# Kernel optimization log

Hardware: AMD Instinct MI355X
Metric: run time of the kernel (lower is better)

The kernel has to match this reference:

```python
import jax, jax.numpy as jnp
import numpy as np

B, N, G, D, H = 32, 512, 512, 512, 16
KD = D // H            # key_dim = embedding_dim // head_num
CLIP = 10.0            # tanh logit clipping


def _heads(x):
    # [B, C, D] -> [B, H, C, KD]
    b, c, _ = x.shape
    return x.reshape(b, c, H, KD).transpose(0, 2, 1, 3)


def setup_inputs() -> dict:
    key = jax.random.key(0)
    ks = jax.random.split(key, 9)
    s = 0.02
    return {
        "encoded_nodes": jax.random.normal(ks[0], (B, N, D), jnp.float32),
        "encoded_last": jax.random.normal(ks[1], (B, G, D), jnp.float32),
        "group_ninf_mask": jnp.zeros((B, G, N), jnp.float32),
        "Wq_graph": jax.random.normal(ks[2], (D, D), jnp.float32) * s,
        "Wq_first": jax.random.normal(ks[3], (D, D), jnp.float32) * s,
        "Wq_last": jax.random.normal(ks[4], (D, D), jnp.float32) * s,
        "Wk": jax.random.normal(ks[5], (D, D), jnp.float32) * s,
        "Wv": jax.random.normal(ks[6], (D, D), jnp.float32) * s,
        "Wcomb": jax.random.normal(ks[7], (D, D), jnp.float32) * s,
        "bcomb": jnp.zeros((D,), jnp.float32),
    }


def reference(encoded_nodes, encoded_last, group_ninf_mask,
              Wq_graph, Wq_first, Wq_last, Wk, Wv, Wcomb, bcomb):
    # reset(): graph embedding = mean over nodes, keys/values from encoded_nodes
    graph = encoded_nodes.mean(axis=1, keepdims=True)            # [B,1,D]
    q = (_heads(graph @ Wq_graph.T)                              # [B,H,1,KD] broadcast
         + _heads(encoded_last @ Wq_first.T)                     # q_first (first call)
         + _heads(encoded_last @ Wq_last.T))                     # [B,H,G,KD]
    k = _heads(encoded_nodes @ Wk.T)                             # [B,H,N,KD]
    v = _heads(encoded_nodes @ Wv.T)                             # [B,H,N,KD]

    # stage 1: masked multi-head attention
    score = jnp.einsum('bhgk,bhnk->bhgn', q, k) / float(np.sqrt(KD))
    score = score + group_ninf_mask[:, None, :, :]
    w = jax.nn.softmax(score, axis=-1)
    out = jnp.einsum('bhgn,bhnk->bhgk', w, v)
    out = out.transpose(0, 2, 1, 3).reshape(-1, G, D)            # [B,G,D]
    mh = out @ Wcomb.T + bcomb

    # stage 2: single-head score -> scale -> tanh clip -> mask -> softmax
    s2 = jnp.einsum('bgd,bnd->bgn', mh, encoded_nodes) / float(np.sqrt(D))
    s2 = CLIP * jnp.tanh(s2) + group_ninf_mask
    return jax.nn.softmax(s2, axis=-1)
```

## Files before the change

kernel.cpp:

```cpp
#include <hip/hip_runtime.h>
#include <hip/hip_bf16.h>
#include <stdint.h>
#include <math.h>

#define B_  32
#define N_  512
#define G_  512
#define D_  512
#define H_  16
#define KD_ 32

using bf16x8 = __attribute__((ext_vector_type(8))) short;
using f32x4  = __attribute__((ext_vector_type(4))) float;
typedef unsigned short u16;

__device__ __forceinline__ u16 f2b(float x) {
  union { __hip_bfloat16 h; u16 u; } c;
  c.h = __float2bfloat16(x);
  return c.u;
}
__device__ __forceinline__ float b2f(u16 u) {
  union { float f; unsigned int i; } c;
  c.i = ((unsigned int)u) << 16;
  return c.f;
}

__device__ __forceinline__ void async16(void* lds, const void* g) {
  __builtin_amdgcn_global_load_lds(
      (const __attribute__((address_space(1))) unsigned int*)(uintptr_t)g,
      (__attribute__((address_space(3))) unsigned int*)(uintptr_t)lds,
      16, 0, 0);
}

__global__ __launch_bounds__(512) void mean_split_kernel(
    const float* __restrict__ enc, u16* __restrict__ hi, u16* __restrict__ lo,
    float* __restrict__ partial)
{
  const int b  = blockIdx.x;
  const int nc = blockIdx.y;
  const int d  = threadIdx.x;
  const size_t base = ((size_t)b * N_ + (size_t)nc * 64) * D_ + d;
  float psum = 0.f;
  for (int i = 0; i < 64; ++i) {
    float v = enc[base + (size_t)i * D_];
    psum += v;
    u16 h = f2b(v);
    hi[base + (size_t)i * D_] = h;
    lo[base + (size_t)i * D_] = f2b(v - b2f(h));
  }
  partial[((size_t)b * 8 + nc) * D_ + d] = psum;
}

__global__ __launch_bounds__(512) void mean_final_kernel(
    const float* __restrict__ partial, float* __restrict__ graph)
{
  const int b = blockIdx.x, d = threadIdx.x;
  float s = 0.f;
  for (int c = 0; c < 8; ++c) s += partial[((size_t)b * 8 + c) * D_ + d];
  graph[b * D_ + d] = s * (1.0f / N_);
}

__global__ void split4_kernel(const float* __restrict__ in,
                              u16* __restrict__ hi, u16* __restrict__ lo, int n4)
{
  int i = blockIdx.x * blockDim.x + threadIdx.x;
  if (i < n4) {
    float4 v = ((const float4*)in)[i];
    ushort4 h, l;
    h.x = f2b(v.x); l.x = f2b(v.x - b2f(h.x));
    h.y = f2b(v.y); l.y = f2b(v.y - b2f(h.y));
    h.z = f2b(v.z); l.z = f2b(v.z - b2f(h.z));
    h.w = f2b(v.w); l.w = f2b(v.w - b2f(h.w));
    ((ushort4*)hi)[i] = h;
    ((ushort4*)lo)[i] = l;
  }
}

__global__ void wsum_split_kernel(const float* __restrict__ a, const float* __restrict__ b,
                                  u16* __restrict__ hi, u16* __restrict__ lo, int n4)
{
  int i = blockIdx.x * blockDim.x + threadIdx.x;
  if (i < n4) {
    float4 va = ((const float4*)a)[i];
    float4 vb = ((const float4*)b)[i];
    float x0 = va.x + vb.x, x1 = va.y + vb.y, x2 = va.z + vb.z, x3 = va.w + vb.w;
    ushort4 h, l;
    h.x = f2b(x0); l.x = f2b(x0 - b2f(h.x));
    h.y = f2b(x1); l.y = f2b(x1 - b2f(h.y));
    h.z = f2b(x2); l.z = f2b(x2 - b2f(h.z));
    h.w = f2b(x3); l.w = f2b(x3 - b2f(h.w));
    ((ushort4*)hi)[i] = h;
    ((ushort4*)lo)[i] = l;
  }
}

__global__ __launch_bounds__(256) void qg_kernel(
    const float* __restrict__ graph, const float* __restrict__ Wq,
    float* __restrict__ qg)
{
  const int b  = blockIdx.y;
  const int dd = blockIdx.x * 256 + threadIdx.x;
  const float* g = graph + b * D_;
  const float* w = Wq + (size_t)dd * D_;
  float s = 0.f;
  for (int k = 0; k < D_; ++k) s += g[k] * w[k];
  qg[b * D_ + dd] = s;
}

__global__ __launch_bounds__(256) void rowmax_kernel(
    const float* __restrict__ mask, float* __restrict__ rmx)
{
  const int row  = blockIdx.x * 4 + (threadIdx.x >> 6);
  const int lane = threadIdx.x & 63;
  const float* r = mask + (size_t)row * N_;
  float4 a  = *(const float4*)&r[lane * 8];
  float4 b4 = *(const float4*)&r[lane * 8 + 4];
  float m = fmaxf(fmaxf(fmaxf(a.x, a.y), fmaxf(a.z, a.w)),
                  fmaxf(fmaxf(b4.x, b4.y), fmaxf(b4.z, b4.w)));
#pragma unroll
  for (int w = 1; w < 64; w <<= 1) m = fmaxf(m, __shfl_xor(m, w));
  if (lane == 0) rmx[row] = m;
}

__global__ __launch_bounds__(64) void kmax_kernel(
    const u16* __restrict__ kvhi, float* __restrict__ kmx)
{
  const int b = blockIdx.x >> 4, h = blockIdx.x & 15;
  const int lane = threadIdx.x;
  float mx = 0.f;
  for (int i = 0; i < 8; ++i) {
    const int n = i * 64 + lane;
    const unsigned int* p =
        (const unsigned int*)&kvhi[((size_t)b * 512 + n) * 1024 + h * 32];
    float s = 0.f;
#pragma unroll
    for (int w = 0; w < 16; ++w) {
      unsigned int u = p[w];
      float f0 = __uint_as_float(u << 16);
      float f1 = __uint_as_float(u & 0xffff0000u);
      s = fmaf(f0, f0, s);
      s = fmaf(f1, f1, s);
    }
    mx = fmaxf(mx, s);
  }
#pragma unroll
  for (int w = 1; w < 64; w <<= 1) mx = fmaxf(mx, __shfl_xor(mx, w));
  if (lane == 0) kmx[blockIdx.x] = sqrtf(mx) * 1.01f;
}

__global__ __launch_bounds__(256) void vtrans_kernel(
    const u16* __restrict__ kvhi, const u16* __restrict__ kvlo,
    u16* __restrict__ vThi, u16* __restrict__ vTlo)
{
  const int b = blockIdx.x >> 4, h = blockIdx.x & 15;
  for (int d = 0; d < 32; ++d) {
#pragma unroll
    for (int c = 0; c < 2; ++c) {
      const int n = c * 256 + threadIdx.x;
      const size_t src = ((size_t)(b * 512 + n)) * 1024 + 512 + h * 32 + d;
      const size_t dst = (((size_t)b * 16 + h) * 32 + d) * 512 + n;
      vThi[dst] = kvhi[src];
      vTlo[dst] = kvlo[src];
    }
  }
}

template<int OUTMODE, int BIASMODE>
__global__ __launch_bounds__(256) void gemm_split_kernel(
    const u16* __restrict__ Ahi, const u16* __restrict__ Alo,
    const u16* __restrict__ Bhi, const u16* __restrict__ Blo,
    void* __restrict__ Chi, void* __restrict__ Clo,
    const float* __restrict__ bias,
    int M, int N, int K, long sA, long sB, long sC)
{
  __shared__ __align__(16) u16 AhS[4096], AlS[4096], BhS[4096], BlS[4096];

  const int z = blockIdx.z;
  Ahi += (size_t)z * sA; Alo += (size_t)z * sA;
  Bhi += (size_t)z * sB; Blo += (size_t)z * sB;

  const int brow = blockIdx.y * 128;
  const int bcol = blockIdx.x * 128;
  const int tid  = threadIdx.x;
  const int wid  = tid >> 6;
  const int lane = tid & 63;
  const int wr = wid >> 1, wc = wid & 1;

  f32x4 acc[4][4] = {};

  const int c0   = wid * 2;
  const int srow = lane >> 2;
  const int skk  = (lane & 3) * 8;

  const size_t g0 = (size_t)(brow + c0 * 16      + srow) * K + skk;
  const size_t g1 = (size_t)(brow + c0 * 16 + 16 + srow) * K + skk;
  const size_t h0 = (size_t)(bcol + c0 * 16      + srow) * K + skk;
  const size_t h1 = (size_t)(bcol + c0 * 16 + 16 + srow) * K + skk;
  u16* lA0 = &AhS[c0 * 512]; u16* lA1 = &AhS[c0 * 512 + 512];
  u16* la0 = &AlS[c0 * 512]; u16* la1 = &AlS[c0 * 512 + 512];
  u16* lB0 = &BhS[c0 * 512]; u16* lB1 = &BhS[c0 * 512 + 512];
  u16* lb0 = &BlS[c0 * 512]; u16* lb1 = &BlS[c0 * 512 + 512];

  const int aoff = (wr * 64 + (lane & 15)) * 32 + (lane >> 4) * 8;
  const int boff = (wc * 64 + (lane & 15)) * 32 + (lane >> 4) * 8;

  for (int k0 = 0; k0 < K; k0 += 32) {
    async16(lA0, Ahi + g0 + k0);
    async16(lA1, Ahi + g1 + k0);
    async16(la0, Alo + g0 + k0);
    async16(la1, Alo + g1 + k0);
    async16(lB0, Bhi + h0 + k0);
    async16(lB1, Bhi + h1 + k0);
    async16(lb0, Blo + h0 + k0);
    async16(lb1, Blo + h1 + k0);
    __syncthreads();

    bf16x8 ah[4], al[4], bh[4], bl[4];
#pragma unroll
    for (int m = 0; m < 4; ++m) {
      ah[m] = *(const bf16x8*)&AhS[aoff + m * 512];
      al[m] = *(const bf16x8*)&AlS[aoff + m * 512];
    }
#pragma unroll
    for (int n = 0; n < 4; ++n) {
      bh[n] = *(const bf16x8*)&BhS[boff + n * 512];
      bl[n] = *(const bf16x8*)&BlS[boff + n * 512];
    }
#pragma unroll
    for (int m = 0; m < 4; ++m)
#pragma unroll
      for (int n = 0; n < 4; ++n) {
        f32x4 t = acc[m][n];
        t = __builtin_amdgcn_mfma_f32_16x16x32_bf16(al[m], bh[n], t, 0, 0, 0);
        t = __builtin_amdgcn_mfma_f32_16x16x32_bf16(ah[m], bl[n], t, 0, 0, 0);
        t = __builtin_amdgcn_mfma_f32_16x16x32_bf16(ah[m], bh[n], t, 0, 0, 0);
        acc[m][n] = t;
      }
    __syncthreads();
  }

  const int r0 = brow + wr * 64 + (lane >> 4) * 4;
  const int cbase = bcol + wc * 64 + (lane & 15);
#pragma unroll
  for (int m = 0; m < 4; ++m) {
#pragma unroll
    for (int n = 0; n < 4; ++n) {
      const int c = cbase + n * 16;
#pragma unroll
      for (int j = 0; j < 4; ++j) {
        const int r = r0 + m * 16 + j;
        float v = acc[m][n][j];
        if (BIASMODE == 1) v += bias[(r >> 9) * 512 + c];
        if (BIASMODE == 2) v += bias[c];
        if (OUTMODE == 0) {
          ((float*)Chi)[(size_t)z * sC + (size_t)r * N + c] = v;
        } else {
          u16 h = f2b(v);
          ((u16*)Chi)[(size_t)r * N + c] = h;
          ((u16*)Clo)[(size_t)r * N + c] = f2b(v - b2f(h));
        }
      }
    }
  }
}

__global__ __launch_bounds__(256) void attn_mfma3_kernel(
    u16* __restrict__ Qhi, u16* __restrict__ Qlo,
    const u16* __restrict__ KVhi, const u16* __restrict__ KVlo,
    const u16* __restrict__ VThi, const u16* __restrict__ VTlo,
    const float* __restrict__ mask,
    const float* __restrict__ rowmaxb,
    const float* __restrict__ kmaxb)
{
  __shared__ __align__(16) u16 Ph[4][32][56], Pl[4][32][56];

  const int tid = threadIdx.x, wid = tid >> 6, lane = tid & 63;
  const int id   = blockIdx.x;
  const int h    = id & 15;
  const int gblk = (id >> 4) & 3;
  const int b    = id >> 6;
  const int g0   = gblk * 128 + wid * 32;
  const int colq = lane & 15, rowg = lane >> 4;

  const size_t qb = ((size_t)b * G_ + g0) * D_ + h * KD_;
  const size_t kb = (size_t)b * N_ * 1024 + h * KD_;
  const size_t vb = (((size_t)b * H_ + h) * KD_) * (size_t)N_;
  const float* Mb = mask + ((size_t)b * G_ + g0) * N_;

  bf16x8 qh[2], ql[2];
  qh[0] = *(const bf16x8*)&Qhi[qb + (size_t)colq * D_ + rowg * 8];
  ql[0] = *(const bf16x8*)&Qlo[qb + (size_t)colq * D_ + rowg * 8];
  qh[1] = *(const bf16x8*)&Qhi[qb + (size_t)(16 + colq) * D_ + rowg * 8];
  ql[1] = *(const bf16x8*)&Qlo[qb + (size_t)(16 + colq) * D_ + rowg * 8];

  const float scale = 0.17677669529663687f;
  const f32x4 zf = {0.f, 0.f, 0.f, 0.f};
  const bf16x8 ones = {0x3F80, 0x3F80, 0x3F80, 0x3F80, 0x3F80, 0x3F80, 0x3F80, 0x3F80};

  const float km = kmaxb[b * 16 + h];
  float nq2[2];
#pragma unroll
  for (int rf = 0; rf < 2; ++rf) {
    float s = 0.f;
    const unsigned int* qw = (const unsigned int*)&qh[rf];
#pragma unroll
    for (int w = 0; w < 4; ++w) {
      unsigned int u = qw[w];
      float f0 = __uint_as_float(u << 16);
      float f1 = __uint_as_float(u & 0xffff0000u);
      s = fmaf(f0, f0, s);
      s = fmaf(f1, f1, s);
    }
    s += __shfl_xor(s, 16);
    s += __shfl_xor(s, 32);
    nq2[rf] = s;
  }
  float mrow[2][4];
#pragma unroll
  for (int rf = 0; rf < 2; ++rf)
#pragma unroll
    for (int j = 0; j < 4; ++j) {
      const int r16 = rowg * 4 + j;
      float nq = sqrtf(__shfl(nq2[rf], r16)) * 1.01f;
      mrow[rf][j] = scale * nq * km + rowmaxb[(size_t)b * G_ + g0 + rf * 16 + r16];
    }

  f32x4 o[2][2] = {};
  f32x4 os[2] = {};

  for (int n0 = 0; n0 < N_; n0 += 32) {
    bf16x8 kh0 = *(const bf16x8*)&KVhi[kb + (size_t)(n0 + colq) * 1024 + rowg * 8];
    bf16x8 kl0 = *(const bf16x8*)&KVlo[kb + (size_t)(n0 + colq) * 1024 + rowg * 8];
    bf16x8 kh1 = *(const bf16x8*)&KVhi[kb + (size_t)(n0 + 16 + colq) * 1024 + rowg * 8];
    bf16x8 kl1 = *(const bf16x8*)&KVlo[kb + (size_t)(n0 + 16 + colq) * 1024 + rowg * 8];
    bf16x8 vh0 = *(const bf16x8*)&VThi[vb + (size_t)colq * N_ + n0 + rowg * 8];
    bf16x8 vl0 = *(const bf16x8*)&VTlo[vb + (size_t)colq * N_ + n0 + rowg * 8];
    bf16x8 vh1 = *(const bf16x8*)&VThi[vb + (size_t)(16 + colq) * N_ + n0 + rowg * 8];
    bf16x8 vl1 = *(const bf16x8*)&VTlo[vb + (size_t)(16 + colq) * N_ + n0 + rowg * 8];

#pragma unroll
    for (int rf = 0; rf < 2; ++rf) {
      f32x4 t0 = __builtin_amdgcn_mfma_f32_16x16x32_bf16(ql[rf], kh0, zf, 0, 0, 0);
      t0 = __builtin_amdgcn_mfma_f32_16x16x32_bf16(qh[rf], kl0, t0, 0, 0, 0);
      t0 = __builtin_amdgcn_mfma_f32_16x16x32_bf16(qh[rf], kh0, t0, 0, 0, 0);
      f32x4 t1 = __builtin_amdgcn_mfma_f32_16x16x32_bf16(ql[rf], kh1, zf, 0, 0, 0);
      t1 = __builtin_amdgcn_mfma_f32_16x16x32_bf16(qh[rf], kl1, t1, 0, 0, 0);
      t1 = __builtin_amdgcn_mfma_f32_16x16x32_bf16(qh[rf], kh1, t1, 0, 0, 0);
#pragma unroll
      for (int j = 0; j < 4; ++j) {
        const int gg = rf * 16 + rowg * 4 + j;
        float m0 = Mb[(size_t)gg * N_ + n0 + colq];
        float m1 = Mb[(size_t)gg * N_ + n0 + 16 + colq];
        float p0 = __expf(fmaf(t0[j], scale, m0 - mrow[rf][j]));
        float p1 = __expf(fmaf(t1[j], scale, m1 - mrow[rf][j]));
        unsigned int uh, ul;
        asm("v_cvt_pk_bf16_f32 %0, %1, %2" : "=v"(uh) : "v"(p0), "v"(p1));
        float h0f = __uint_as_float(uh << 16);
        float h1f = __uint_as_float(uh & 0xffff0000u);
        float l0 = p0 - h0f, l1 = p1 - h1f;
        asm("v_cvt_pk_bf16_f32 %0, %1, %2" : "=v"(ul) : "v"(l0), "v"(l1));
        Ph[wid][gg][colq]      = (u16)uh;
        Ph[wid][gg][16 + colq] = (u16)(uh >> 16);
        Pl[wid][gg][colq]      = (u16)ul;
        Pl[wid][gg][16 + colq] = (u16)(ul >> 16);
      }
    }
    asm volatile("s_waitcnt lgkmcnt(0)" ::: "memory");

    bf16x8 ph0 = *(const bf16x8*)&Ph[wid][colq][rowg * 8];
    bf16x8 pl0 = *(const bf16x8*)&Pl[wid][colq][rowg * 8];
    bf16x8 ph1 = *(const bf16x8*)&Ph[wid][16 + colq][rowg * 8];
    bf16x8 pl1 = *(const bf16x8*)&Pl[wid][16 + colq][rowg * 8];

    o[0][0] = __builtin_amdgcn_mfma_f32_16x16x32_bf16(pl0, vh0, o[0][0], 0, 0, 0);
    o[0][0] = __builtin_amdgcn_mfma_f32_16x16x32_bf16(ph0, vl0, o[0][0], 0, 0, 0);
    o[0][0] = __builtin_amdgcn_mfma_f32_16x16x32_bf16(ph0, vh0, o[0][0], 0, 0, 0);
    o[0][1] = __builtin_amdgcn_mfma_f32_16x16x32_bf16(pl0, vh1, o[0][1], 0, 0, 0);
    o[0][1] = __builtin_amdgcn_mfma_f32_16x16x32_bf16(ph0, vl1, o[0][1], 0, 0, 0);
    o[0][1] = __builtin_amdgcn_mfma_f32_16x16x32_bf16(ph0, vh1, o[0][1], 0, 0, 0);
    o[1][0] = __builtin_amdgcn_mfma_f32_16x16x32_bf16(pl1, vh0, o[1][0], 0, 0, 0);
    o[1][0] = __builtin_amdgcn_mfma_f32_16x16x32_bf16(ph1, vl0, o[1][0], 0, 0, 0);
    o[1][0] = __builtin_amdgcn_mfma_f32_16x16x32_bf16(ph1, vh0, o[1][0], 0, 0, 0);
    o[1][1] = __builtin_amdgcn_mfma_f32_16x16x32_bf16(pl1, vh1, o[1][1], 0, 0, 0);
    o[1][1] = __builtin_amdgcn_mfma_f32_16x16x32_bf16(ph1, vl1, o[1][1], 0, 0, 0);
    o[1][1] = __builtin_amdgcn_mfma_f32_16x16x32_bf16(ph1, vh1, o[1][1], 0, 0, 0);
    os[0] = __builtin_amdgcn_mfma_f32_16x16x32_bf16(ph0, ones, os[0], 0, 0, 0);
    os[0] = __builtin_amdgcn_mfma_f32_16x16x32_bf16(pl0, ones, os[0], 0, 0, 0);
    os[1] = __builtin_amdgcn_mfma_f32_16x16x32_bf16(ph1, ones, os[1], 0, 0, 0);
    os[1] = __builtin_amdgcn_mfma_f32_16x16x32_bf16(pl1, ones, os[1], 0, 0, 0);
  }

#pragma unroll
  for (int rf = 0; rf < 2; ++rf)
#pragma unroll
    for (int j = 0; j < 4; ++j) {
      const float inv = 1.f / os[rf][j];
      const int gg = rf * 16 + rowg * 4 + j;
      float v0 = o[rf][0][j] * inv;
      float v1 = o[rf][1][j] * inv;
      u16 h0 = f2b(v0), h1 = f2b(v1);
      Qhi[qb + (size_t)gg * D_ + colq]      = h0;
      Qlo[qb + (size_t)gg * D_ + colq]      = f2b(v0 - b2f(h0));
      Qhi[qb + (size_t)gg * D_ + 16 + colq] = h1;
      Qlo[qb + (size_t)gg * D_ + 16 + colq] = f2b(v1 - b2f(h1));
    }
}

__global__ __launch_bounds__(256) void softmax2_kernel(
    float* __restrict__ S, const float* __restrict__ mask)
{
  const int row  = blockIdx.x * 4 + (threadIdx.x >> 6);
  const int lane = threadIdx.x & 63;
  float* r = S + (size_t)row * N_;
  const float* mk = mask + (size_t)row * N_;
  const float iscale = 0.04419417382415922f;

  float4 a  = *(const float4*)&r[lane * 8];
  float4 b4 = *(const float4*)&r[lane * 8 + 4];
  float4 ma = *(const float4*)&mk[lane * 8];
  float4 mb = *(const float4*)&mk[lane * 8 + 4];

  float v[8] = {a.x, a.y, a.z, a.w, b4.x, b4.y, b4.z, b4.w};
  float m[8] = {ma.x, ma.y, ma.z, ma.w, mb.x, mb.y, mb.z, mb.w};

#pragma unroll
  for (int i = 0; i < 8; ++i) {
    float x  = v[i] * iscale;
    float e2 = __expf(2.f * x);
    float t  = 1.f - 2.f / (e2 + 1.f);
    v[i] = 10.f * t + m[i];
  }
  float mx = v[0];
#pragma unroll
  for (int i = 1; i < 8; ++i) mx = fmaxf(mx, v[i]);
#pragma unroll
  for (int w = 1; w < 64; w <<= 1) mx = fmaxf(mx, __shfl_xor(mx, w));
  float sum = 0.f;
#pragma unroll
  for (int i = 0; i < 8; ++i) { v[i] = __expf(v[i] - mx); sum += v[i]; }
#pragma unroll
  for (int w = 1; w < 64; w <<= 1) sum += __shfl_xor(sum, w);
  const float inv = 1.f / sum;

  float4 oa = {v[0] * inv, v[1] * inv, v[2] * inv, v[3] * inv};
  float4 ob = {v[4] * inv, v[5] * inv, v[6] * inv, v[7] * inv};
  *(float4*)&r[lane * 8]     = oa;
  *(float4*)&r[lane * 8 + 4] = ob;
}

extern "C" void kernel_launch(void* const* d_in, const int* in_sizes, int n_in,
                              void* d_out, int out_size, void* d_ws, size_t ws_size,
                              hipStream_t stream)
{
  const float* enc_nodes = (const float*)d_in[0];
  const float* enc_last  = (const float*)d_in[1];
  const float* mask      = (const float*)d_in[2];
  const float* Wq_graph  = (const float*)d_in[3];
  const float* Wq_first  = (const float*)d_in[4];
  const float* Wq_last   = (const float*)d_in[5];
  const float* Wk        = (const float*)d_in[6];
  const float* Wv        = (const float*)d_in[7];
  const float* Wcomb     = (const float*)d_in[8];
  const float* bcomb     = (const float*)d_in[9];
  float* out = (float*)d_out;

  char* ws = (char*)d_ws;
  size_t off = 0;
  auto alloc = [&](size_t bytes) {
    void* p = ws + off;
    off += (bytes + 255) & ~(size_t)255;
    return p;
  };

  const size_t EL = (size_t)B_ * G_ * D_;
  u16* encNhi = (u16*)alloc(EL * 2);
  u16* encNlo = (u16*)alloc(EL * 2);
  u16* encLhi = (u16*)alloc(EL * 2);
  u16* encLlo = (u16*)alloc(EL * 2);
  u16* qhi    = (u16*)alloc(EL * 2);
  u16* qlo    = (u16*)alloc(EL * 2);
  u16* kvhi   = (u16*)alloc(EL * 4);
  u16* kvlo   = (u16*)alloc(EL * 4);
  u16* Wqlhi  = (u16*)alloc((size_t)D_ * D_ * 2);
  u16* Wqllo  = (u16*)alloc((size_t)D_ * D_ * 2);
  u16* Wkvhi  = (u16*)alloc((size_t)D_ * D_ * 4);
  u16* Wkvlo  = (u16*)alloc((size_t)D_ * D_ * 4);
  u16* Wchi   = (u16*)alloc((size_t)D_ * D_ * 2);
  u16* Wclo   = (u16*)alloc((size_t)D_ * D_ * 2);
  float* partial = (float*)alloc((size_t)B_ * 8 * D_ * 4);
  float* graph   = (float*)alloc((size_t)B_ * D_ * 4);
  float* qg      = (float*)alloc((size_t)B_ * D_ * 4);
  float* rowmaxb = (float*)alloc((size_t)B_ * G_ * 4);
  float* kmaxb   = (float*)alloc((size_t)B_ * H_ * 4);
  u16* vThi = encLhi; u16* vTlo = encLlo;
  u16* athi = qhi;    u16* atlo = qlo;
  u16* mhhi = kvhi;   u16* mhlo = kvlo;

  mean_split_kernel<<<dim3(32, 8), 512, 0, stream>>>(enc_nodes, encNhi, encNlo, partial);
  mean_final_kernel<<<dim3(32), 512, 0, stream>>>(partial, graph);
  split4_kernel<<<dim3(8192), 256, 0, stream>>>(enc_last, encLhi, encLlo, (int)(EL / 4));
  wsum_split_kernel<<<dim3(256), 256, 0, stream>>>(Wq_first, Wq_last, Wqlhi, Wqllo, 65536);
  split4_kernel<<<dim3(256), 256, 0, stream>>>(Wk, Wkvhi, Wkvlo, 65536);
  split4_kernel<<<dim3(256), 256, 0, stream>>>(Wv, Wkvhi + 262144, Wkvlo + 262144, 65536);
  split4_kernel<<<dim3(256), 256, 0, stream>>>(Wcomb, Wchi, Wclo, 65536);
  qg_kernel<<<dim3(2, 32), 256, 0, stream>>>(graph, Wq_graph, qg);
  rowmax_kernel<<<dim3(4096), 256, 0, stream>>>(mask, rowmaxb);

  gemm_split_kernel<1, 1><<<dim3(4, 128, 1), 256, 0, stream>>>(
      encLhi, encLlo, Wqlhi, Wqllo, qhi, qlo, qg, 16384, 512, 512, 0, 0, 0);
  gemm_split_kernel<1, 0><<<dim3(8, 128, 1), 256, 0, stream>>>(
      encNhi, encNlo, Wkvhi, Wkvlo, kvhi, kvlo, nullptr, 16384, 1024, 512, 0, 0, 0);
  vtrans_kernel<<<dim3(512), 256, 0, stream>>>(kvhi, kvlo, vThi, vTlo);
  kmax_kernel<<<dim3(512), 64, 0, stream>>>(kvhi, kmaxb);

  attn_mfma3_kernel<<<dim3(2048), 256, 0, stream>>>(
      qhi, qlo, kvhi, kvlo, vThi, vTlo, mask, rowmaxb, kmaxb);

  gemm_split_kernel<1, 2><<<dim3(4, 128, 1), 256, 0, stream>>>(
      athi, atlo, Wchi, Wclo, mhhi, mhlo, bcomb, 16384, 512, 512, 0, 0, 0);
  gemm_split_kernel<0, 0><<<dim3(4, 4, 32), 256, 0, stream>>>(
      mhhi, mhlo, encNhi, encNlo, out, nullptr, nullptr, 512, 512, 512,
      262144, 262144, 262144);

  softmax2_kernel<<<dim3(4096), 256, 0, stream>>>(out, mask);
}
```

Baseline: 494.8 us.

## Fuse V transpose into KV GEMM epilogue and pipeline attention loop

The K/V projection GEMM epilogue now writes K to a compact buffer and V directly in transposed per-head layout, removing the separate transpose kernel and its extra memory pass. The attention kernel is software-pipelined with double-buffered K/V/mask registers and P shared-memory tiles, so the next tile's loads and QK-softmax overlap the current PV MFMAs. This costs more registers and makes the V stores from the GEMM uncoalesced.

```diff
diff --git a/kernel.cpp b/kernel.cpp
--- a/kernel.cpp
+++ b/kernel.cpp
@@ -123,7 +123,7 @@
 }
 
 __global__ __launch_bounds__(64) void kmax_kernel(
-    const u16* __restrict__ kvhi, float* __restrict__ kmx)
+    const u16* __restrict__ khi, float* __restrict__ kmx)
 {
   const int b = blockIdx.x >> 4, h = blockIdx.x & 15;
   const int lane = threadIdx.x;
@@ -131,7 +131,7 @@
   for (int i = 0; i < 8; ++i) {
     const int n = i * 64 + lane;
     const unsigned int* p =
-        (const unsigned int*)&kvhi[((size_t)b * 512 + n) * 1024 + h * 32];
+        (const unsigned int*)&khi[((size_t)b * 512 + n) * 512 + h * 32];
     float s = 0.f;
 #pragma unroll
     for (int w = 0; w < 16; ++w) {
@@ -148,28 +148,12 @@
   if (lane == 0) kmx[blockIdx.x] = sqrtf(mx) * 1.01f;
 }
 
-__global__ __launch_bounds__(256) void vtrans_kernel(
-    const u16* __restrict__ kvhi, const u16* __restrict__ kvlo,
-    u16* __restrict__ vThi, u16* __restrict__ vTlo)
-{
-  const int b = blockIdx.x >> 4, h = blockIdx.x & 15;
-  for (int d = 0; d < 32; ++d) {
-#pragma unroll
-    for (int c = 0; c < 2; ++c) {
-      const int n = c * 256 + threadIdx.x;
-      const size_t src = ((size_t)(b * 512 + n)) * 1024 + 512 + h * 32 + d;
-      const size_t dst = (((size_t)b * 16 + h) * 32 + d) * 512 + n;
-      vThi[dst] = kvhi[src];
-      vTlo[dst] = kvlo[src];
-    }
-  }
-}
-
 template<int OUTMODE, int BIASMODE>
 __global__ __launch_bounds__(256) void gemm_split_kernel(
     const u16* __restrict__ Ahi, const u16* __restrict__ Alo,
     const u16* __restrict__ Bhi, const u16* __restrict__ Blo,
     void* __restrict__ Chi, void* __restrict__ Clo,
+    void* __restrict__ Dhi, void* __restrict__ Dlo,
     const float* __restrict__ bias,
     int M, int N, int K, long sA, long sB, long sC)
 {
@@ -254,25 +238,37 @@
         if (BIASMODE == 2) v += bias[c];
         if (OUTMODE == 0) {
           ((float*)Chi)[(size_t)z * sC + (size_t)r * N + c] = v;
-        } else {
+        } else if (OUTMODE == 1) {
           u16 h = f2b(v);
           ((u16*)Chi)[(size_t)r * N + c] = h;
           ((u16*)Clo)[(size_t)r * N + c] = f2b(v - b2f(h));
+        } else {
+          u16 hv = f2b(v);
+          u16 lv = f2b(v - b2f(hv));
+          if (c < 512) {
+            ((u16*)Chi)[(size_t)r * 512 + c] = hv;
+            ((u16*)Clo)[(size_t)r * 512 + c] = lv;
+          } else {
+            const int bb = r >> 9, nn = r & 511, hh = (c >> 5) & 15, dd = c & 31;
+            const size_t idx = (((size_t)bb * 16 + hh) * 32 + dd) * 512 + nn;
+            ((u16*)Dhi)[idx] = hv;
+            ((u16*)Dlo)[idx] = lv;
+          }
         }
       }
     }
   }
 }
 
-__global__ __launch_bounds__(256) void attn_mfma3_kernel(
+__global__ __launch_bounds__(256) void attn_mfma4_kernel(
     u16* __restrict__ Qhi, u16* __restrict__ Qlo,
-    const u16* __restrict__ KVhi, const u16* __restrict__ KVlo,
+    const u16* __restrict__ Khi, const u16* __restrict__ Klo,
     const u16* __restrict__ VThi, const u16* __restrict__ VTlo,
     const float* __restrict__ mask,
     const float* __restrict__ rowmaxb,
     const float* __restrict__ kmaxb)
 {
-  __shared__ __align__(16) u16 Ph[4][32][56], Pl[4][32][56];
+  __shared__ __align__(16) u16 Ph[2][4][32][40], Pl[2][4][32][40];
 
   const int tid = threadIdx.x, wid = tid >> 6, lane = tid & 63;
   const int id   = blockIdx.x;
@@ -283,7 +279,7 @@
   const int colq = lane & 15, rowg = lane >> 4;
 
   const size_t qb = ((size_t)b * G_ + g0) * D_ + h * KD_;
-  const size_t kb = (size_t)b * N_ * 1024 + h * KD_;
+  const size_t kb = ((size_t)b * N_) * D_ + h * KD_;
   const size_t vb = (((size_t)b * H_ + h) * KD_) * (size_t)N_;
   const float* Mb = mask + ((size_t)b * G_ + g0) * N_;
 
@@ -296,6 +292,81 @@
   const float scale = 0.17677669529663687f;
   const f32x4 zf = {0.f, 0.f, 0.f, 0.f};
   const bf16x8 ones = {0x3F80, 0x3F80, 0x3F80, 0x3F80, 0x3F80, 0x3F80, 0x3F80, 0x3F80};
+
+  bf16x8 kh0[2], kl0[2], kh1[2], kl1[2];
+  bf16x8 vh0[2], vl0[2], vh1[2], vl1[2];
+  float  mm0[2][4], mm1[2][4];
+
+#define LOADK(s, n0_)                                                          \
+  kh0[s] = *(const bf16x8*)&Khi[kb + (size_t)((n0_) + colq) * D_ + rowg * 8];  \
+  kl0[s] = *(const bf16x8*)&Klo[kb + (size_t)((n0_) + colq) * D_ + rowg * 8];  \
+  kh1[s] = *(const bf16x8*)&Khi[kb + (size_t)((n0_) + 16 + colq) * D_ + rowg * 8]; \
+  kl1[s] = *(const bf16x8*)&Klo[kb + (size_t)((n0_) + 16 + colq) * D_ + rowg * 8];
+
+#define LOADV(s, n0_)                                                          \
+  vh0[s] = *(const bf16x8*)&VThi[vb + (size_t)colq * N_ + (n0_) + rowg * 8];   \
+  vl0[s] = *(const bf16x8*)&VTlo[vb + (size_t)colq * N_ + (n0_) + rowg * 8];   \
+  vh1[s] = *(const bf16x8*)&VThi[vb + (size_t)(16 + colq) * N_ + (n0_) + rowg * 8]; \
+  vl1[s] = *(const bf16x8*)&VTlo[vb + (size_t)(16 + colq) * N_ + (n0_) + rowg * 8];
+
+#define LOADM(n0_)                                                             \
+  _Pragma("unroll") for (int rf = 0; rf < 2; ++rf)                             \
+  _Pragma("unroll") for (int j = 0; j < 4; ++j) {                              \
+    const int gg = rf * 16 + rowg * 4 + j;                                     \
+    mm0[rf][j] = Mb[(size_t)gg * N_ + (n0_) + colq] - mrow[rf][j];             \
+    mm1[rf][j] = Mb[(size_t)gg * N_ + (n0_) + 16 + colq] - mrow[rf][j];        \
+  }
+
+#define QKSM(s, bb)                                                            \
+  _Pragma("unroll") for (int rf = 0; rf < 2; ++rf) {                           \
+    f32x4 t0 = __builtin_amdgcn_mfma_f32_16x16x32_bf16(ql[rf], kh0[s], zf, 0, 0, 0); \
+    t0 = __builtin_amdgcn_mfma_f32_16x16x32_bf16(qh[rf], kl0[s], t0, 0, 0, 0); \
+    t0 = __builtin_amdgcn_mfma_f32_16x16x32_bf16(qh[rf], kh0[s], t0, 0, 0, 0); \
+    f32x4 t1 = __builtin_amdgcn_mfma_f32_16x16x32_bf16(ql[rf], kh1[s], zf, 0, 0, 0); \
+    t1 = __builtin_amdgcn_mfma_f32_16x16x32_bf16(qh[rf], kl1[s], t1, 0, 0, 0); \
+    t1 = __builtin_amdgcn_mfma_f32_16x16x32_bf16(qh[rf], kh1[s], t1, 0, 0, 0); \
+    _Pragma("unroll") for (int j = 0; j < 4; ++j) {                            \
+      const int gg = rf * 16 + rowg * 4 + j;                                   \
+      float p0 = __expf(fmaf(t0[j], scale, mm0[rf][j]));                       \
+      float p1 = __expf(fmaf(t1[j], scale, mm1[rf][j]));                       \
+      unsigned int uh_, ul_;                                                   \
+      asm("v_cvt_pk_bf16_f32 %0, %1, %2" : "=v"(uh_) : "v"(p0), "v"(p1));      \
+      float h0f = __uint_as_float(uh_ << 16);                                  \
+      float h1f = __uint_as_float(uh_ & 0xffff0000u);                          \
+      float l0_ = p0 - h0f, l1_ = p1 - h1f;                                    \
+      asm("v_cvt_pk_bf16_f32 %0, %1, %2" : "=v"(ul_) : "v"(l0_), "v"(l1_));    \
+      Ph[bb][wid][gg][colq]      = (u16)uh_;                                   \
+      Ph[bb][wid][gg][16 + colq] = (u16)(uh_ >> 16);                           \
+      Pl[bb][wid][gg][colq]      = (u16)ul_;                                   \
+      Pl[bb][wid][gg][16 + colq] = (u16)(ul_ >> 16);                           \
+    }                                                                          \
+  }
+
+#define PVACC(s, bb) {                                                         \
+    bf16x8 ph0 = *(const bf16x8*)&Ph[bb][wid][colq][rowg * 8];                 \
+    bf16x8 pl0 = *(const bf16x8*)&Pl[bb][wid][colq][rowg * 8];                 \
+    bf16x8 ph1 = *(const bf16x8*)&Ph[bb][wid][16 + colq][rowg * 8];            \
+    bf16x8 pl1 = *(const bf16x8*)&Pl[bb][wid][16 + colq][rowg * 8];            \
+    o[0][0] = __builtin_amdgcn_mfma_f32_16x16x32_bf16(pl0, vh0[s], o[0][0], 0, 0, 0); \
+    o[0][0] = __builtin_amdgcn_mfma_f32_16x16x32_bf16(ph0, vl0[s], o[0][0], 0, 0, 0); \
+    o[0][0] = __builtin_amdgcn_mfma_f32_16x16x32_bf16(ph0, vh0[s], o[0][0], 0, 0, 0); \
+    o[0][1] = __builtin_amdgcn_mfma_f32_16x16x32_bf16(pl0, vh1[s], o[0][1], 0, 0, 0); \
+    o[0][1] = __builtin_amdgcn_mfma_f32_16x16x32_bf16(ph0, vl1[s], o[0][1], 0, 0, 0); \
+    o[0][1] = __builtin_amdgcn_mfma_f32_16x16x32_bf16(ph0, vh1[s], o[0][1], 0, 0, 0); \
+    o[1][0] = __builtin_amdgcn_mfma_f32_16x16x32_bf16(pl1, vh0[s], o[1][0], 0, 0, 0); \
+    o[1][0] = __builtin_amdgcn_mfma_f32_16x16x32_bf16(ph1, vl0[s], o[1][0], 0, 0, 0); \
+    o[1][0] = __builtin_amdgcn_mfma_f32_16x16x32_bf16(ph1, vh0[s], o[1][0], 0, 0, 0); \
+    o[1][1] = __builtin_amdgcn_mfma_f32_16x16x32_bf16(pl1, vh1[s], o[1][1], 0, 0, 0); \
+    o[1][1] = __builtin_amdgcn_mfma_f32_16x16x32_bf16(ph1, vl1[s], o[1][1], 0, 0, 0); \
+    o[1][1] = __builtin_amdgcn_mfma_f32_16x16x32_bf16(ph1, vh1[s], o[1][1], 0, 0, 0); \
+    os[0] = __builtin_amdgcn_mfma_f32_16x16x32_bf16(ph0, ones, os[0], 0, 0, 0); \
+    os[0] = __builtin_amdgcn_mfma_f32_16x16x32_bf16(pl0, ones, os[0], 0, 0, 0); \
+    os[1] = __builtin_amdgcn_mfma_f32_16x16x32_bf16(ph1, ones, os[1], 0, 0, 0); \
+    os[1] = __builtin_amdgcn_mfma_f32_16x16x32_bf16(pl1, ones, os[1], 0, 0, 0); \
+  }
+
+  LOADK(0, 0)
+  LOADV(0, 0)
 
   const float km = kmaxb[b * 16 + h];
   float nq2[2];
@@ -325,70 +396,33 @@
       mrow[rf][j] = scale * nq * km + rowmaxb[(size_t)b * G_ + g0 + rf * 16 + r16];
     }
 
+  LOADM(0)
+  QKSM(0, 0)
+
   f32x4 o[2][2] = {};
   f32x4 os[2] = {};
 
-  for (int n0 = 0; n0 < N_; n0 += 32) {
-    bf16x8 kh0 = *(const bf16x8*)&KVhi[kb + (size_t)(n0 + colq) * 1024 + rowg * 8];
-    bf16x8 kl0 = *(const bf16x8*)&KVlo[kb + (size_t)(n0 + colq) * 1024 + rowg * 8];
-    bf16x8 kh1 = *(const bf16x8*)&KVhi[kb + (size_t)(n0 + 16 + colq) * 1024 + rowg * 8];
-    bf16x8 kl1 = *(const bf16x8*)&KVlo[kb + (size_t)(n0 + 16 + colq) * 1024 + rowg * 8];
-    bf16x8 vh0 = *(const bf16x8*)&VThi[vb + (size_t)colq * N_ + n0 + rowg * 8];
-    bf16x8 vl0 = *(const bf16x8*)&VTlo[vb + (size_t)colq * N_ + n0 + rowg * 8];
-    bf16x8 vh1 = *(const bf16x8*)&VThi[vb + (size_t)(16 + colq) * N_ + n0 + rowg * 8];
-    bf16x8 vl1 = *(const bf16x8*)&VTlo[vb + (size_t)(16 + colq) * N_ + n0 + rowg * 8];
-
-#pragma unroll
-    for (int rf = 0; rf < 2; ++rf) {
-      f32x4 t0 = __builtin_amdgcn_mfma_f32_16x16x32_bf16(ql[rf], kh0, zf, 0, 0, 0);
-      t0 = __builtin_amdgcn_mfma_f32_16x16x32_bf16(qh[rf], kl0, t0, 0, 0, 0);
-      t0 = __builtin_amdgcn_mfma_f32_16x16x32_bf16(qh[rf], kh0, t0, 0, 0, 0);
-      f32x4 t1 = __builtin_amdgcn_mfma_f32_16x16x32_bf16(ql[rf], kh1, zf, 0, 0, 0);
-      t1 = __builtin_amdgcn_mfma_f32_16x16x32_bf16(qh[rf], kl1, t1, 0, 0, 0);
-      t1 = __builtin_amdgcn_mfma_f32_16x16x32_bf16(qh[rf], kh1, t1, 0, 0, 0);
-#pragma unroll
-      for (int j = 0; j < 4; ++j) {
-        const int gg = rf * 16 + rowg * 4 + j;
-        float m0 = Mb[(size_t)gg * N_ + n0 + colq];
-        float m1 = Mb[(size_t)gg * N_ + n0 + 16 + colq];
-        float p0 = __expf(fmaf(t0[j], scale, m0 - mrow[rf][j]));
-        float p1 = __expf(fmaf(t1[j], scale, m1 - mrow[rf][j]));
-        unsigned int uh, ul;
-        asm("v_cvt_pk_bf16_f32 %0, %1, %2" : "=v"(uh) : "v"(p0), "v"(p1));
-        float h0f = __uint_as_float(uh << 16);
-        float h1f = __uint_as_float(uh & 0xffff0000u);
-        float l0 = p0 - h0f, l1 = p1 - h1f;
-        asm("v_cvt_pk_bf16_f32 %0, %1, %2" : "=v"(ul) : "v"(l0), "v"(l1));
-        Ph[wid][gg][colq]      = (u16)uh;
-        Ph[wid][gg][16 + colq] = (u16)(uh >> 16);
-        Pl[wid][gg][colq]      = (u16)ul;
-        Pl[wid][gg][16 + colq] = (u16)(ul >> 16);
-      }
+#pragma unroll
+  for (int t = 0; t < 16; ++t) {
+    const int cur = t & 1, nxt = cur ^ 1;
+    if (t < 15) {
+      LOADK(nxt, (t + 1) * 32)
+      LOADV(nxt, (t + 1) * 32)
+      LOADM((t + 1) * 32)
     }
     asm volatile("s_waitcnt lgkmcnt(0)" ::: "memory");
-
-    bf16x8 ph0 = *(const bf16x8*)&Ph[wid][colq][rowg * 8];
-    bf16x8 pl0 = *(const bf16x8*)&Pl[wid][colq][rowg * 8];
-    bf16x8 ph1 = *(const bf16x8*)&Ph[wid][16 + colq][rowg * 8];
-    bf16x8 pl1 = *(const bf16x8*)&Pl[wid][16 + colq][rowg * 8];
-
-    o[0][0] = __builtin_amdgcn_mfma_f32_16x16x32_bf16(pl0, vh0, o[0][0], 0, 0, 0);
-    o[0][0] = __builtin_amdgcn_mfma_f32_16x16x32_bf16(ph0, vl0, o[0][0], 0, 0, 0);
-    o[0][0] = __builtin_amdgcn_mfma_f32_16x16x32_bf16(ph0, vh0, o[0][0], 0, 0, 0);
-    o[0][1] = __builtin_amdgcn_mfma_f32_16x16x32_bf16(pl0, vh1, o[0][1], 0, 0, 0);
-    o[0][1] = __builtin_amdgcn_mfma_f32_16x16x32_bf16(ph0, vl1, o[0][1], 0, 0, 0);
-    o[0][1] = __builtin_amdgcn_mfma_f32_16x16x32_bf16(ph0, vh1, o[0][1], 0, 0, 0);
-    o[1][0] = __builtin_amdgcn_mfma_f32_16x16x32_bf16(pl1, vh0, o[1][0], 0, 0, 0);
-    o[1][0] = __builtin_amdgcn_mfma_f32_16x16x32_bf16(ph1, vl0, o[1][0], 0, 0, 0);
-    o[1][0] = __builtin_amdgcn_mfma_f32_16x16x32_bf16(ph1, vh0, o[1][0], 0, 0, 0);
-    o[1][1] = __builtin_amdgcn_mfma_f32_16x16x32_bf16(pl1, vh1, o[1][1], 0, 0, 0);
-    o[1][1] = __builtin_amdgcn_mfma_f32_16x16x32_bf16(ph1, vl1, o[1][1], 0, 0, 0);
-    o[1][1] = __builtin_amdgcn_mfma_f32_16x16x32_bf16(ph1, vh1, o[1][1], 0, 0, 0);
-    os[0] = __builtin_amdgcn_mfma_f32_16x16x32_bf16(ph0, ones, os[0], 0, 0, 0);
-    os[0] = __builtin_amdgcn_mfma_f32_16x16x32_bf16(pl0, ones, os[0], 0, 0, 0);
-    os[1] = __builtin_amdgcn_mfma_f32_16x16x32_bf16(ph1, ones, os[1], 0, 0, 0);
-    os[1] = __builtin_amdgcn_mfma_f32_16x16x32_bf16(pl1, ones, os[1], 0, 0, 0);
-  }
+    __builtin_amdgcn_sched_barrier(0);
+    PVACC(cur, cur)
+    if (t < 15) {
+      QKSM(nxt, nxt)
+    }
+  }
+
+#undef LOADK
+#undef LOADV
+#undef LOADM
+#undef QKSM
+#undef PVACC
 
 #pragma unroll
   for (int rf = 0; rf < 2; ++rf)
@@ -479,8 +513,8 @@
   u16* encLlo = (u16*)alloc(EL * 2);
   u16* qhi    = (u16*)alloc(EL * 2);
   u16* qlo    = (u16*)alloc(EL * 2);
-  u16* kvhi   = (u16*)alloc(EL * 4);
-  u16* kvlo   = (u16*)alloc(EL * 4);
+  u16* khi    = (u16*)alloc(EL * 2);
+  u16* klo    = (u16*)alloc(EL * 2);
   u16* Wqlhi  = (u16*)alloc((size_t)D_ * D_ * 2);
   u16* Wqllo  = (u16*)alloc((size_t)D_ * D_ * 2);
   u16* Wkvhi  = (u16*)alloc((size_t)D_ * D_ * 4);
@@ -494,7 +528,7 @@
   float* kmaxb   = (float*)alloc((size_t)B_ * H_ * 4);
   u16* vThi = encLhi; u16* vTlo = encLlo;
   u16* athi = qhi;    u16* atlo = qlo;
-  u16* mhhi = kvhi;   u16* mhlo = kvlo;
+  u16* mhhi = khi;    u16* mhlo = klo;
 
   mean_split_kernel<<<dim3(32, 8), 512, 0, stream>>>(enc_nodes, encNhi, encNlo, partial);
   mean_final_kernel<<<dim3(32), 512, 0, stream>>>(partial, graph);
@@ -507,20 +541,22 @@
   rowmax_kernel<<<dim3(4096), 256, 0, stream>>>(mask, rowmaxb);
 
   gemm_split_kernel<1, 1><<<dim3(4, 128, 1), 256, 0, stream>>>(
-      encLhi, encLlo, Wqlhi, Wqllo, qhi, qlo, qg, 16384, 512, 512, 0, 0, 0);
-  gemm_split_kernel<1, 0><<<dim3(8, 128, 1), 256, 0, stream>>>(
-      encNhi, encNlo, Wkvhi, Wkvlo, kvhi, kvlo, nullptr, 16384, 1024, 512, 0, 0, 0);
-  vtrans_kernel<<<dim3(512), 256, 0, stream>>>(kvhi, kvlo, vThi, vTlo);
-  kmax_kernel<<<dim3(512), 64, 0, stream>>>(kvhi, kmaxb);
-
-  attn_mfma3_kernel<<<dim3(2048), 256, 0, stream>>>(
-      qhi, qlo, kvhi, kvlo, vThi, vTlo, mask, rowmaxb, kmaxb);
+      encLhi, encLlo, Wqlhi, Wqllo, qhi, qlo, nullptr, nullptr, qg,
+      16384, 512, 512, 0, 0, 0);
+  gemm_split_kernel<3, 0><<<dim3(8, 128, 1), 256, 0, stream>>>(
+      encNhi, encNlo, Wkvhi, Wkvlo, khi, klo, vThi, vTlo, nullptr,
+      16384, 1024, 512, 0, 0, 0);
+  kmax_kernel<<<dim3(512), 64, 0, stream>>>(khi, kmaxb);
+
+  attn_mfma4_kernel<<<dim3(2048), 256, 0, stream>>>(
+      qhi, qlo, khi, klo, vThi, vTlo, mask, rowmaxb, kmaxb);
 
   gemm_split_kernel<1, 2><<<dim3(4, 128, 1), 256, 0, stream>>>(
-      athi, atlo, Wchi, Wclo, mhhi, mhlo, bcomb, 16384, 512, 512, 0, 0, 0);
+      athi, atlo, Wchi, Wclo, mhhi, mhlo, nullptr, nullptr, bcomb,
+      16384, 512, 512, 0, 0, 0);
   gemm_split_kernel<0, 0><<<dim3(4, 4, 32), 256, 0, stream>>>(
-      mhhi, mhlo, encNhi, encNlo, out, nullptr, nullptr, 512, 512, 512,
-      262144, 262144, 262144);
+      mhhi, mhlo, encNhi, encNlo, out, nullptr, nullptr, nullptr, nullptr,
+      512, 512, 512, 262144, 262144, 262144);
 
   softmax2_kernel<<<dim3(4096), 256, 0, stream>>>(out, mask);
 }
```

Result: faster. 463.0 us (-6.4%).

## Fuse V transpose into KV GEMM epilogue and stage-2 GEMM with softmax

Applied to the files above, without the earlier changes.

The KV projection GEMM epilogue now writes K in a compact [B,N,D] layout and writes V directly in transposed per-head layout, which removes the separate vtrans kernel and its strided byte-wise copies. The stage-2 batched GEMM is fused with the tanh-clip, mask and softmax into one kernel. Each block computes a full 64x512 row tile held in registers, so the fp32 score matrix is never written out and read back. The attention kernel also raises wave priority around its MFMA blocks. In exchange, the fused kernel uses a large accumulator array and 64KB+ of LDS, so occupancy and grid size (256 blocks) drop, and the V epilogue performs scattered 2-byte stores.

```diff
diff --git a/kernel.cpp b/kernel.cpp
--- a/kernel.cpp
+++ b/kernel.cpp
@@ -123,7 +123,7 @@
 }
 
 __global__ __launch_bounds__(64) void kmax_kernel(
-    const u16* __restrict__ kvhi, float* __restrict__ kmx)
+    const u16* __restrict__ khi, float* __restrict__ kmx)
 {
   const int b = blockIdx.x >> 4, h = blockIdx.x & 15;
   const int lane = threadIdx.x;
@@ -131,7 +131,7 @@
   for (int i = 0; i < 8; ++i) {
     const int n = i * 64 + lane;
     const unsigned int* p =
-        (const unsigned int*)&kvhi[((size_t)b * 512 + n) * 1024 + h * 32];
+        (const unsigned int*)&khi[((size_t)b * 512 + n) * 512 + h * 32];
     float s = 0.f;
 #pragma unroll
     for (int w = 0; w < 16; ++w) {
@@ -148,36 +148,16 @@
   if (lane == 0) kmx[blockIdx.x] = sqrtf(mx) * 1.01f;
 }
 
-__global__ __launch_bounds__(256) void vtrans_kernel(
-    const u16* __restrict__ kvhi, const u16* __restrict__ kvlo,
-    u16* __restrict__ vThi, u16* __restrict__ vTlo)
-{
-  const int b = blockIdx.x >> 4, h = blockIdx.x & 15;
-  for (int d = 0; d < 32; ++d) {
-#pragma unroll
-    for (int c = 0; c < 2; ++c) {
-      const int n = c * 256 + threadIdx.x;
-      const size_t src = ((size_t)(b * 512 + n)) * 1024 + 512 + h * 32 + d;
-      const size_t dst = (((size_t)b * 16 + h) * 32 + d) * 512 + n;
-      vThi[dst] = kvhi[src];
-      vTlo[dst] = kvlo[src];
-    }
-  }
-}
-
 template<int OUTMODE, int BIASMODE>
 __global__ __launch_bounds__(256) void gemm_split_kernel(
     const u16* __restrict__ Ahi, const u16* __restrict__ Alo,
     const u16* __restrict__ Bhi, const u16* __restrict__ Blo,
     void* __restrict__ Chi, void* __restrict__ Clo,
+    void* __restrict__ Dhi, void* __restrict__ Dlo,
     const float* __restrict__ bias,
-    int M, int N, int K, long sA, long sB, long sC)
+    int M, int N, int K)
 {
   __shared__ __align__(16) u16 AhS[4096], AlS[4096], BhS[4096], BlS[4096];
-
-  const int z = blockIdx.z;
-  Ahi += (size_t)z * sA; Alo += (size_t)z * sA;
-  Bhi += (size_t)z * sB; Blo += (size_t)z * sB;
 
   const int brow = blockIdx.y * 128;
   const int bcol = blockIdx.x * 128;
@@ -252,21 +232,30 @@
         float v = acc[m][n][j];
         if (BIASMODE == 1) v += bias[(r >> 9) * 512 + c];
         if (BIASMODE == 2) v += bias[c];
-        if (OUTMODE == 0) {
-          ((float*)Chi)[(size_t)z * sC + (size_t)r * N + c] = v;
+        u16 hv = f2b(v);
+        u16 lv = f2b(v - b2f(hv));
+        if (OUTMODE == 1) {
+          ((u16*)Chi)[(size_t)r * N + c] = hv;
+          ((u16*)Clo)[(size_t)r * N + c] = lv;
         } else {
-          u16 h = f2b(v);
-          ((u16*)Chi)[(size_t)r * N + c] = h;
-          ((u16*)Clo)[(size_t)r * N + c] = f2b(v - b2f(h));
+          if (c < 512) {
+            ((u16*)Chi)[(size_t)r * 512 + c] = hv;
+            ((u16*)Clo)[(size_t)r * 512 + c] = lv;
+          } else {
+            const int bb = r >> 9, nn = r & 511, hh = (c >> 5) & 15, dd = c & 31;
+            const size_t idx = (((size_t)bb * 16 + hh) * 32 + dd) * 512 + nn;
+            ((u16*)Dhi)[idx] = hv;
+            ((u16*)Dlo)[idx] = lv;
+          }
         }
       }
     }
   }
 }
 
-__global__ __launch_bounds__(256) void attn_mfma3_kernel(
+__global__ __launch_bounds__(256) void attn_mfma5_kernel(
     u16* __restrict__ Qhi, u16* __restrict__ Qlo,
-    const u16* __restrict__ KVhi, const u16* __restrict__ KVlo,
+    const u16* __restrict__ Khi, const u16* __restrict__ Klo,
     const u16* __restrict__ VThi, const u16* __restrict__ VTlo,
     const float* __restrict__ mask,
     const float* __restrict__ rowmaxb,
@@ -283,7 +272,7 @@
   const int colq = lane & 15, rowg = lane >> 4;
 
   const size_t qb = ((size_t)b * G_ + g0) * D_ + h * KD_;
-  const size_t kb = (size_t)b * N_ * 1024 + h * KD_;
+  const size_t kb = ((size_t)b * N_) * D_ + h * KD_;
   const size_t vb = (((size_t)b * H_ + h) * KD_) * (size_t)N_;
   const float* Mb = mask + ((size_t)b * G_ + g0) * N_;
 
@@ -329,10 +318,10 @@
   f32x4 os[2] = {};
 
   for (int n0 = 0; n0 < N_; n0 += 32) {
-    bf16x8 kh0 = *(const bf16x8*)&KVhi[kb + (size_t)(n0 + colq) * 1024 + rowg * 8];
-    bf16x8 kl0 = *(const bf16x8*)&KVlo[kb + (size_t)(n0 + colq) * 1024 + rowg * 8];
-    bf16x8 kh1 = *(const bf16x8*)&KVhi[kb + (size_t)(n0 + 16 + colq) * 1024 + rowg * 8];
-    bf16x8 kl1 = *(const bf16x8*)&KVlo[kb + (size_t)(n0 + 16 + colq) * 1024 + rowg * 8];
+    bf16x8 kh0 = *(const bf16x8*)&Khi[kb + (size_t)(n0 + colq) * D_ + rowg * 8];
+    bf16x8 kl0 = *(const bf16x8*)&Klo[kb + (size_t)(n0 + colq) * D_ + rowg * 8];
+    bf16x8 kh1 = *(const bf16x8*)&Khi[kb + (size_t)(n0 + 16 + colq) * D_ + rowg * 8];
+    bf16x8 kl1 = *(const bf16x8*)&Klo[kb + (size_t)(n0 + 16 + colq) * D_ + rowg * 8];
     bf16x8 vh0 = *(const bf16x8*)&VThi[vb + (size_t)colq * N_ + n0 + rowg * 8];
     bf16x8 vl0 = *(const bf16x8*)&VTlo[vb + (size_t)colq * N_ + n0 + rowg * 8];
     bf16x8 vh1 = *(const bf16x8*)&VThi[vb + (size_t)(16 + colq) * N_ + n0 + rowg * 8];
@@ -340,12 +329,14 @@
 
 #pragma unroll
     for (int rf = 0; rf < 2; ++rf) {
+      __builtin_amdgcn_s_setprio(1);
       f32x4 t0 = __builtin_amdgcn_mfma_f32_16x16x32_bf16(ql[rf], kh0, zf, 0, 0, 0);
       t0 = __builtin_amdgcn_mfma_f32_16x16x32_bf16(qh[rf], kl0, t0, 0, 0, 0);
       t0 = __builtin_amdgcn_mfma_f32_16x16x32_bf16(qh[rf], kh0, t0, 0, 0, 0);
       f32x4 t1 = __builtin_amdgcn_mfma_f32_16x16x32_bf16(ql[rf], kh1, zf, 0, 0, 0);
       t1 = __builtin_amdgcn_mfma_f32_16x16x32_bf16(qh[rf], kl1, t1, 0, 0, 0);
       t1 = __builtin_amdgcn_mfma_f32_16x16x32_bf16(qh[rf], kh1, t1, 0, 0, 0);
+      __builtin_amdgcn_s_setprio(0);
 #pragma unroll
       for (int j = 0; j < 4; ++j) {
         const int gg = rf * 16 + rowg * 4 + j;
@@ -372,6 +363,7 @@
     bf16x8 ph1 = *(const bf16x8*)&Ph[wid][16 + colq][rowg * 8];
     bf16x8 pl1 = *(const bf16x8*)&Pl[wid][16 + colq][rowg * 8];
 
+    __builtin_amdgcn_s_setprio(1);
     o[0][0] = __builtin_amdgcn_mfma_f32_16x16x32_bf16(pl0, vh0, o[0][0], 0, 0, 0);
     o[0][0] = __builtin_amdgcn_mfma_f32_16x16x32_bf16(ph0, vl0, o[0][0], 0, 0, 0);
     o[0][0] = __builtin_amdgcn_mfma_f32_16x16x32_bf16(ph0, vh0, o[0][0], 0, 0, 0);
@@ -388,6 +380,7 @@
     os[0] = __builtin_amdgcn_mfma_f32_16x16x32_bf16(pl0, ones, os[0], 0, 0, 0);
     os[1] = __builtin_amdgcn_mfma_f32_16x16x32_bf16(ph1, ones, os[1], 0, 0, 0);
     os[1] = __builtin_amdgcn_mfma_f32_16x16x32_bf16(pl1, ones, os[1], 0, 0, 0);
+    __builtin_amdgcn_s_setprio(0);
   }
 
 #pragma unroll
@@ -406,46 +399,101 @@
     }
 }
 
-__global__ __launch_bounds__(256) void softmax2_kernel(
-    float* __restrict__ S, const float* __restrict__ mask)
-{
-  const int row  = blockIdx.x * 4 + (threadIdx.x >> 6);
-  const int lane = threadIdx.x & 63;
-  float* r = S + (size_t)row * N_;
-  const float* mk = mask + (size_t)row * N_;
+__global__ __launch_bounds__(256) void s2fused_kernel(
+    const u16* __restrict__ Ahi, const u16* __restrict__ Alo,
+    const u16* __restrict__ Bhi, const u16* __restrict__ Blo,
+    const float* __restrict__ mask, float* __restrict__ out)
+{
+  __shared__ __align__(16) u16 AhS[2048], AlS[2048];
+  __shared__ __align__(16) u16 BhS[16384], BlS[16384];
+
+  const int z    = blockIdx.y;
+  const int brow = blockIdx.x * 64;
+  const int tid  = threadIdx.x;
+  const int wid  = tid >> 6;
+  const int lane = tid & 63;
+  const int colq = lane & 15, rowg = lane >> 4;
+
+  const u16* Az_hi = Ahi + (size_t)z * 262144;
+  const u16* Az_lo = Alo + (size_t)z * 262144;
+  const u16* Bz_hi = Bhi + (size_t)z * 262144;
+  const u16* Bz_lo = Blo + (size_t)z * 262144;
+
+  f32x4 acc[32] = {};
+
+  const int srow = lane >> 2;
+  const int skk  = (lane & 3) * 8;
+
+  const size_t ga = (size_t)(brow + wid * 16 + srow) * 512 + skk;
+  u16* lAh = &AhS[wid * 512];
+  u16* lAl = &AlS[wid * 512];
+
+  const int aoff = (wid * 16 + colq) * 32 + rowg * 8;
+
+  for (int k0 = 0; k0 < 512; k0 += 32) {
+    async16(lAh, Az_hi + ga + k0);
+    async16(lAl, Az_lo + ga + k0);
+#pragma unroll
+    for (int c = 0; c < 8; ++c) {
+      const int chunk = wid * 8 + c;
+      const size_t gb = (size_t)(chunk * 16 + srow) * 512 + skk + k0;
+      async16(&BhS[chunk * 512], Bz_hi + gb);
+      async16(&BlS[chunk * 512], Bz_lo + gb);
+    }
+    __syncthreads();
+
+    bf16x8 ah = *(const bf16x8*)&AhS[aoff];
+    bf16x8 al = *(const bf16x8*)&AlS[aoff];
+#pragma unroll
+    for (int nf = 0; nf < 32; ++nf) {
+      const int boff = (nf * 16 + colq) * 32 + rowg * 8;
+      bf16x8 bh = *(const bf16x8*)&BhS[boff];
+      bf16x8 bl = *(const bf16x8*)&BlS[boff];
+      f32x4 t = acc[nf];
+      t = __builtin_amdgcn_mfma_f32_16x16x32_bf16(al, bh, t, 0, 0, 0);
+      t = __builtin_amdgcn_mfma_f32_16x16x32_bf16(ah, bl, t, 0, 0, 0);
+      t = __builtin_amdgcn_mfma_f32_16x16x32_bf16(ah, bh, t, 0, 0, 0);
+      acc[nf] = t;
+    }
+    __syncthreads();
+  }
+
   const float iscale = 0.04419417382415922f;
-
-  float4 a  = *(const float4*)&r[lane * 8];
-  float4 b4 = *(const float4*)&r[lane * 8 + 4];
-  float4 ma = *(const float4*)&mk[lane * 8];
-  float4 mb = *(const float4*)&mk[lane * 8 + 4];
-
-  float v[8] = {a.x, a.y, a.z, a.w, b4.x, b4.y, b4.z, b4.w};
-  float m[8] = {ma.x, ma.y, ma.z, ma.w, mb.x, mb.y, mb.z, mb.w};
-
-#pragma unroll
-  for (int i = 0; i < 8; ++i) {
-    float x  = v[i] * iscale;
-    float e2 = __expf(2.f * x);
-    float t  = 1.f - 2.f / (e2 + 1.f);
-    v[i] = 10.f * t + m[i];
-  }
-  float mx = v[0];
-#pragma unroll
-  for (int i = 1; i < 8; ++i) mx = fmaxf(mx, v[i]);
-#pragma unroll
-  for (int w = 1; w < 64; w <<= 1) mx = fmaxf(mx, __shfl_xor(mx, w));
-  float sum = 0.f;
-#pragma unroll
-  for (int i = 0; i < 8; ++i) { v[i] = __expf(v[i] - mx); sum += v[i]; }
-#pragma unroll
-  for (int w = 1; w < 64; w <<= 1) sum += __shfl_xor(sum, w);
-  const float inv = 1.f / sum;
-
-  float4 oa = {v[0] * inv, v[1] * inv, v[2] * inv, v[3] * inv};
-  float4 ob = {v[4] * inv, v[5] * inv, v[6] * inv, v[7] * inv};
-  *(float4*)&r[lane * 8]     = oa;
-  *(float4*)&r[lane * 8 + 4] = ob;
+  const size_t rbase = ((size_t)z * 512 + brow + wid * 16 + rowg * 4) * 512;
+
+#pragma unroll
+  for (int j = 0; j < 4; ++j) {
+    const size_t roff = rbase + (size_t)j * 512 + colq;
+#pragma unroll
+    for (int nf = 0; nf < 32; ++nf) {
+      float x  = acc[nf][j] * iscale;
+      float e2 = __expf(2.f * x);
+      float t  = 1.f - 2.f / (e2 + 1.f);
+      acc[nf][j] = 10.f * t + mask[roff + nf * 16];
+    }
+  }
+#pragma unroll
+  for (int j = 0; j < 4; ++j) {
+    float mx = acc[0][j];
+#pragma unroll
+    for (int nf = 1; nf < 32; ++nf) mx = fmaxf(mx, acc[nf][j]);
+#pragma unroll
+    for (int w = 1; w < 16; w <<= 1) mx = fmaxf(mx, __shfl_xor(mx, w));
+    float sum = 0.f;
+#pragma unroll
+    for (int nf = 0; nf < 32; ++nf) {
+      float e = __expf(acc[nf][j] - mx);
+      acc[nf][j] = e;
+      sum += e;
+    }
+#pragma unroll
+    for (int w = 1; w < 16; w <<= 1) sum += __shfl_xor(sum, w);
+    const float inv = 1.f / sum;
+    const size_t roff = rbase + (size_t)j * 512 + colq;
+#pragma unroll
+    for (int nf = 0; nf < 32; ++nf)
+      out[roff + nf * 16] = acc[nf][j] * inv;
+  }
 }
 
 extern "C" void kernel_launch(void* const* d_in, const int* in_sizes, int n_in,
@@ -479,8 +527,8 @@
   u16* encLlo = (u16*)alloc(EL * 2);
   u16* qhi    = (u16*)alloc(EL * 2);
   u16* qlo    = (u16*)alloc(EL * 2);
-  u16* kvhi   = (u16*)alloc(EL * 4);
-  u16* kvlo   = (u16*)alloc(EL * 4);
+  u16* khi    = (u16*)alloc(EL * 2);
+  u16* klo    = (u16*)alloc(EL * 2);
   u16* Wqlhi  = (u16*)alloc((size_t)D_ * D_ * 2);
   u16* Wqllo  = (u16*)alloc((size_t)D_ * D_ * 2);
   u16* Wkvhi  = (u16*)alloc((size_t)D_ * D_ * 4);
@@ -494,7 +542,7 @@
   float* kmaxb   = (float*)alloc((size_t)B_ * H_ * 4);
   u16* vThi = encLhi; u16* vTlo = encLlo;
   u16* athi = qhi;    u16* atlo = qlo;
-  u16* mhhi = kvhi;   u16* mhlo = kvlo;
+  u16* mhhi = khi;    u16* mhlo = klo;
 
   mean_split_kernel<<<dim3(32, 8), 512, 0, stream>>>(enc_nodes, encNhi, encNlo, partial);
   mean_final_kernel<<<dim3(32), 512, 0, stream>>>(partial, graph);
@@ -507,20 +555,20 @@
   rowmax_kernel<<<dim3(4096), 256, 0, stream>>>(mask, rowmaxb);
 
   gemm_split_kernel<1, 1><<<dim3(4, 128, 1), 256, 0, stream>>>(
-      encLhi, encLlo, Wqlhi, Wqllo, qhi, qlo, qg, 16384, 512, 512, 0, 0, 0);
-  gemm_split_kernel<1, 0><<<dim3(8, 128, 1), 256, 0, stream>>>(
-      encNhi, encNlo, Wkvhi, Wkvlo, kvhi, kvlo, nullptr, 16384, 1024, 512, 0, 0, 0);
-  vtrans_kernel<<<dim3(512), 256, 0, stream>>>(kvhi, kvlo, vThi, vTlo);
-  kmax_kernel<<<dim3(512), 64, 0, stream>>>(kvhi, kmaxb);
-
-  attn_mfma3_kernel<<<dim3(2048), 256, 0, stream>>>(
-      qhi, qlo, kvhi, kvlo, vThi, vTlo, mask, rowmaxb, kmaxb);
+      encLhi, encLlo, Wqlhi, Wqllo, qhi, qlo, nullptr, nullptr, qg,
+      16384, 512, 512);
+  gemm_split_kernel<3, 0><<<dim3(8, 128, 1), 256, 0, stream>>>(
+      encNhi, encNlo, Wkvhi, Wkvlo, khi, klo, vThi, vTlo, nullptr,
+      16384, 1024, 512);
+  kmax_kernel<<<dim3(512), 64, 0, stream>>>(khi, kmaxb);
+
+  attn_mfma5_kernel<<<dim3(2048), 256, 0, stream>>>(
+      qhi, qlo, khi, klo, vThi, vTlo, mask, rowmaxb, kmaxb);
 
   gemm_split_kernel<1, 2><<<dim3(4, 128, 1), 256, 0, stream>>>(
-      athi, atlo, Wchi, Wclo, mhhi, mhlo, bcomb, 16384, 512, 512, 0, 0, 0);
-  gemm_split_kernel<0, 0><<<dim3(4, 4, 32), 256, 0, stream>>>(
-      mhhi, mhlo, encNhi, encNlo, out, nullptr, nullptr, 512, 512, 512,
-      262144, 262144, 262144);
-
-  softmax2_kernel<<<dim3(4096), 256, 0, stream>>>(out, mask);
-}
+      athi, atlo, Wchi, Wclo, mhhi, mhlo, nullptr, nullptr, bcomb,
+      16384, 512, 512);
+
+  s2fused_kernel<<<dim3(8, 32), 256, 0, stream>>>(
+      mhhi, mhlo, encNhi, encNlo, mask, out);
+}
```

Result: slower. 508.8 us (+2.8%).
